# Kernel tuning notes

Measured on AMD Instinct MI355X. Metric: run time of the kernel, lower is better.

The kernel has to match this reference:

```python
import jax, jax.numpy as jnp
import numpy as np

B, N, H, L = 8, 256, 128, 3
NF, EF, TD, FH = 6, 15, 4, 64  # node feat, edge feat, temporal dim, flow hidden


def setup_inputs() -> dict:
    key = jax.random.key(0)
    ks = jax.random.split(key, 16)
    s = 0.05
    return {
        "node_features": jax.random.normal(ks[0], (B, N, NF), jnp.float32),
        "edge_features": jax.random.normal(ks[1], (B, N, N, EF), jnp.float32),
        "temporal_features": jax.random.normal(ks[2], (B, N, N, TD), jnp.float32),
        "adjacency": jax.random.randint(ks[3], (N, N), 0, 2, jnp.int32),
        "W_emb": jax.random.normal(ks[4], (NF, H), jnp.float32) * s,
        "b_emb": jnp.zeros((H,), jnp.float32),
        "msg_W": jax.random.normal(ks[5], (L, H + 3, H), jnp.float32) * s,
        "msg_b": jnp.zeros((L, H), jnp.float32),
        "upd_W": jax.random.normal(ks[6], (L, 2 * H, H), jnp.float32) * s,
        "upd_b": jnp.zeros((L, H), jnp.float32),
        "W1": jax.random.normal(ks[7], (2 * H + 3 + TD, FH), jnp.float32) * s,
        "b1": jnp.zeros((FH,), jnp.float32),
        "W2": jax.random.normal(ks[8], (FH, 1), jnp.float32) * s,
        "b2": jnp.zeros((1,), jnp.float32),
    }


def reference(node_features, edge_features, temporal_features, adjacency,
              W_emb, b_emb, msg_W, msg_b, upd_W, upd_b, W1, b1, W2, b2):
    # mask[j, i] = 1 if node i is a neighbor of node j (adjacency[j] > 0)
    mask = (adjacency > 0).astype(node_features.dtype)          # [N, N]
    deg = mask.sum(axis=1)                                      # [N]
    edge_rel = edge_features[..., -3:]                          # [B, N, N, 3]
    # aggregated relation features per destination j: sum_i mask[j,i] * edge_rel[b,i,j,:]
    r_agg = jnp.einsum('ji,bijc->bjc', mask, edge_rel)          # [B, N, 3]

    # node embedding (dropout = identity in eval)
    emb = jax.nn.relu(node_features @ W_emb + b_emb)            # [B, N, H]

    for l in range(L):
        We, Wr = msg_W[l, :H], msg_W[l, H:]                     # [H,H], [3,H]
        # msg_nn is linear, so the masked sum decomposes exactly:
        # messages[b,j] = sum_i mask[j,i]*(emb_i @ We + r_ij @ Wr + b)
        messages = (jnp.einsum('ji,bih->bjh', mask, emb @ We)
                    + r_agg @ Wr
                    + deg[None, :, None] * msg_b[l])            # [B, N, H]
        emb = jax.nn.relu(
            jnp.concatenate([emb, messages], axis=-1) @ upd_W[l] + upd_b[l])

    # pairwise flow MLP, first Linear split by input blocks [emb_i, emb_j, r, t]
    Wi, Wj = W1[:H], W1[H:2 * H]
    Wr1, Wt = W1[2 * H:2 * H + 3], W1[2 * H + 3:]
    hi = emb @ Wi                                               # [B, N, FH]
    hj = emb @ Wj                                               # [B, N, FH]
    h = jax.nn.relu(hi[:, :, None, :] + hj[:, None, :, :]
                    + edge_rel @ Wr1 + temporal_features @ Wt + b1)  # [B,N,N,FH]
    flows = jax.nn.relu(h @ W2 + b2)[..., 0]                    # [B, N, N]
    return flows
```

## Files before the change

kernel.cpp:

```cpp
#include <hip/hip_runtime.h>

#define B 8
#define N 256
#define H 128
#define NF 6
#define EF 15
#define TD 4
#define FH 64
#define M (B*N)

typedef unsigned short u16;
using short8  = __attribute__((ext_vector_type(8))) short;
using short4v = __attribute__((ext_vector_type(4))) short;
using f32x4   = __attribute__((ext_vector_type(4))) float;

__device__ __forceinline__ u16 f2bf(float x) {
    unsigned u = __float_as_uint(x);
    u += 0x7fffu + ((u >> 16) & 1u);
    return (u16)(u >> 16);
}
__device__ __forceinline__ float bf2f(u16 h) {
    return __uint_as_float(((unsigned)h) << 16);
}

__global__ void k_prep(const float* __restrict__ msg_W, const float* __restrict__ upd_W,
                       const float* __restrict__ W1,
                       u16* __restrict__ WeTh, u16* __restrict__ WeTl,
                       u16* __restrict__ UwTh, u16* __restrict__ UwTl,
                       u16* __restrict__ W1Th, u16* __restrict__ W1Tl) {
    int idx = blockIdx.x * 256 + threadIdx.x;
    float v; u16 *dh, *dl; int d;
    if (idx < 3 * 16384) {
        int l = idx / 16384, r = idx & 16383;
        int c = r >> 7, h = r & 127;
        v = msg_W[l * ((H + 3) * H) + h * H + c];
        dh = WeTh; dl = WeTl; d = idx;
    } else if (idx < 3 * 16384 + 3 * 32768) {
        int r0 = idx - 3 * 16384;
        int l = r0 / 32768, r = r0 & 32767;
        int c = r >> 8, k = r & 255;
        v = upd_W[l * (2 * H * H) + k * H + c];
        dh = UwTh; dl = UwTl; d = r0;
    } else {
        int r0 = idx - 3 * 16384 - 3 * 32768;
        int f = r0 >> 8, k = r0 & 255;
        v = W1[k * FH + f];
        dh = W1Th; dl = W1Tl; d = r0;
    }
    u16 h = f2bf(v);
    dh[d] = h;
    dl[d] = f2bf(v - bf2f(h));
}

__global__ __launch_bounds__(512) void k_init(
    const int* __restrict__ adj, const float* __restrict__ nf,
    const float* __restrict__ Wemb, const float* __restrict__ bemb,
    float* __restrict__ deg, float* __restrict__ maskT, float* __restrict__ ragg,
    u16* __restrict__ eRh, u16* __restrict__ eRl,
    u16* __restrict__ eTh, u16* __restrict__ eTl)
{
    __shared__ float red[4];
    __shared__ __align__(16) float sout[16][132];
    int t = threadIdx.x;
    if (blockIdx.x < 256) {
        int x = blockIdx.x;
        if (t < 256) {
            float v = (adj[x * N + t] > 0) ? 1.f : 0.f;
            for (int o = 32; o > 0; o >>= 1) v += __shfl_down(v, o);
            if ((t & 63) == 0) red[t >> 6] = v;
            maskT[x * N + t] = (adj[t * N + x] > 0) ? 1.f : 0.f;
            if (t < 24) ragg[x * 24 + t] = 0.f;
        }
        __syncthreads();
        if (t == 0) deg[x] = red[0] + red[1] + red[2] + red[3];
    } else {
        int tile = blockIdx.x - 256;
        int row = t >> 5, h0 = (t & 31) * 4;
        int gr = tile * 16 + row;
        float xv[NF];
#pragma unroll
        for (int k = 0; k < NF; ++k) xv[k] = nf[gr * NF + k];
#pragma unroll
        for (int c = 0; c < 4; ++c) {
            float a = bemb[h0 + c];
#pragma unroll
            for (int k = 0; k < NF; ++k) a += xv[k] * Wemb[k * H + h0 + c];
            sout[row][h0 + c] = fmaxf(a, 0.f);
        }
        __syncthreads();
        {
            float4 v = *(const float4*)&sout[row][h0];
            short4v ph, pl;
            float xs[4] = {v.x, v.y, v.z, v.w};
#pragma unroll
            for (int c = 0; c < 4; ++c) {
                u16 h = f2bf(xs[c]);
                ph[c] = (short)h;
                pl[c] = (short)f2bf(xs[c] - bf2f(h));
            }
            *(short4v*)&eRh[(size_t)gr * H + h0] = ph;
            *(short4v*)&eRl[(size_t)gr * H + h0] = pl;
        }
        {
            int hh = t >> 2, jj = (t & 3) * 4;
            short4v th, tl;
#pragma unroll
            for (int r = 0; r < 4; ++r) {
                float x = sout[jj + r][hh];
                u16 h = f2bf(x);
                th[r] = (short)h;
                tl[r] = (short)f2bf(x - bf2f(h));
            }
            size_t o = (size_t)(tile >> 4) * H * N + (size_t)hh * N + ((tile & 15) * 16) + jj;
            *(short4v*)&eTh[o] = th;
            *(short4v*)&eTl[o] = tl;
        }
    }
}

__global__ void k_erel(const float* __restrict__ edge, const float* __restrict__ maskT,
                       float* __restrict__ e0p, float* __restrict__ e1p,
                       float* __restrict__ e2p, float* __restrict__ ragg) {
    int blk = blockIdx.x;
    int b = blk >> 5, ic = blk & 31;
    int j = threadIdx.x;
    float r0 = 0.f, r1 = 0.f, r2 = 0.f;
#pragma unroll
    for (int ii = 0; ii < 8; ++ii) {
        int i = ic * 8 + ii;
        size_t base = ((size_t)(b * N + i)) * N + j;
        const float* e = edge + base * EF + (EF - 3);
        float e0 = e[0], e1 = e[1], e2 = e[2];
        e0p[base] = e0; e1p[base] = e1; e2p[base] = e2;
        float m = maskT[i * N + j];
        r0 += m * e0; r1 += m * e1; r2 += m * e2;
    }
    float* r = ragg + ((size_t)(b * N) + j) * 3;
    atomicAdd(r + 0, r0);
    atomicAdd(r + 1, r1);
    atomicAdd(r + 2, r2);
}

template <bool LAST>
__global__ __launch_bounds__(512) void k_layer(
    const u16* __restrict__ embR_hi, const u16* __restrict__ embR_lo,
    const u16* __restrict__ embT_hi, const u16* __restrict__ embT_lo,
    const int* __restrict__ adj, const float* __restrict__ ragg,
    const float* __restrict__ deg,
    const u16* __restrict__ WeT_hi, const u16* __restrict__ WeT_lo,
    const float* __restrict__ mwl, const float* __restrict__ mbl,
    const u16* __restrict__ UwT_hi, const u16* __restrict__ UwT_lo,
    const float* __restrict__ ubl,
    u16* __restrict__ oR_hi, u16* __restrict__ oR_lo,
    u16* __restrict__ oT_hi, u16* __restrict__ oT_lo,
    const u16* __restrict__ W1T_hi, const u16* __restrict__ W1T_lo,
    float* __restrict__ hi_out, float* __restrict__ hj_out)
{
    __shared__ __align__(16) u16 sbt[2][2][128][40];
    __shared__ __align__(16) u16 smask[16][264];
    __shared__ __align__(16) u16 semb_hi[16][136], semb_lo[16][136];
    __shared__ __align__(16) u16 sagg_hi[16][136], sagg_lo[16][136];
    __shared__ __align__(16) u16 smsg_hi[16][136], smsg_lo[16][136];
    __shared__ __align__(16) float sout[16][132];

    const int t = threadIdx.x;
    const int wave = t >> 6, lane = t & 63;
    const int lrow = lane & 15;
    const int kg8  = (lane >> 4) * 8;
    const int rb   = (lane >> 4) * 4;
    const int cb   = wave * 16;
    const int blk  = blockIdx.x;
    const int b    = blk >> 4, tile = blk & 15;
    const int j0   = tile * 16;
    const int gb   = b * N;

    const int sp = t >> 8, task = t & 255;
    const int sh = task >> 2, sseg = (task & 3) * 8;

    short8 r0, r1;

    {
        int j = t >> 5, i0 = (t & 31) * 8;
        int4 a0 = *(const int4*)(adj + (j0 + j) * N + i0);
        int4 a1 = *(const int4*)(adj + (j0 + j) * N + i0 + 4);
        short8 mrow;
        mrow[0] = (a0.x > 0) ? (short)0x3F80 : (short)0;
        mrow[1] = (a0.y > 0) ? (short)0x3F80 : (short)0;
        mrow[2] = (a0.z > 0) ? (short)0x3F80 : (short)0;
        mrow[3] = (a0.w > 0) ? (short)0x3F80 : (short)0;
        mrow[4] = (a1.x > 0) ? (short)0x3F80 : (short)0;
        mrow[5] = (a1.y > 0) ? (short)0x3F80 : (short)0;
        mrow[6] = (a1.z > 0) ? (short)0x3F80 : (short)0;
        mrow[7] = (a1.w > 0) ? (short)0x3F80 : (short)0;
        *(short8*)&smask[j][i0] = mrow;
        int h0 = (t & 31) * 4;
        *(short4v*)&semb_hi[j][h0] = *(const short4v*)&embR_hi[(size_t)(gb + j0 + j) * H + h0];
        *(short4v*)&semb_lo[j][h0] = *(const short4v*)&embR_lo[(size_t)(gb + j0 + j) * H + h0];
    }

    const u16* sA_hi = embT_hi + (size_t)b * H * N;
    const u16* sA_lo = embT_lo + (size_t)b * H * N;

    auto LD = [&](const u16* srcHi, const u16* srcLo, int rs, int ko) {
        const u16* s = sp ? srcLo : srcHi;
        r0 = *(const short8*)(s + (size_t)sh * rs + ko + sseg);
        r1 = *(const short8*)(s + (size_t)(sh + 64) * rs + ko + sseg);
    };
    auto WR = [&](int buf) {
        *(short8*)&sbt[buf][sp][sh][sseg] = r0;
        *(short8*)&sbt[buf][sp][sh + 64][sseg] = r1;
    };

    f32x4 acc = {0.f, 0.f, 0.f, 0.f};
    LD(sA_hi, sA_lo, N, 0);
    WR(0);
    __syncthreads();
    for (int c = 0; c < 8; ++c) {
        if (c < 7) LD(sA_hi, sA_lo, N, (c + 1) * 32);
        short8 am = *(const short8*)&smask[lrow][c * 32 + kg8];
        short8 bh = *(const short8*)&sbt[c & 1][0][cb + lrow][kg8];
        short8 bl = *(const short8*)&sbt[c & 1][1][cb + lrow][kg8];
        acc = __builtin_amdgcn_mfma_f32_16x16x32_bf16(am, bh, acc, 0, 0, 0);
        acc = __builtin_amdgcn_mfma_f32_16x16x32_bf16(am, bl, acc, 0, 0, 0);
        if (c < 7) WR((c + 1) & 1);
        __syncthreads();
    }
#pragma unroll
    for (int r = 0; r < 4; ++r) {
        float v = acc[r];
        u16 h = f2bf(v);
        sagg_hi[rb + r][cb + lrow] = h;
        sagg_lo[rb + r][cb + lrow] = f2bf(v - bf2f(h));
    }

    acc = (f32x4){0.f, 0.f, 0.f, 0.f};
    LD(WeT_hi, WeT_lo, H, 0);
    WR(0);
    __syncthreads();
    for (int c = 0; c < 4; ++c) {
        if (c < 3) LD(WeT_hi, WeT_lo, H, (c + 1) * 32);
        short8 ah = *(const short8*)&sagg_hi[lrow][c * 32 + kg8];
        short8 al = *(const short8*)&sagg_lo[lrow][c * 32 + kg8];
        short8 bh = *(const short8*)&sbt[c & 1][0][cb + lrow][kg8];
        short8 bl = *(const short8*)&sbt[c & 1][1][cb + lrow][kg8];
        acc = __builtin_amdgcn_mfma_f32_16x16x32_bf16(ah, bh, acc, 0, 0, 0);
        acc = __builtin_amdgcn_mfma_f32_16x16x32_bf16(ah, bl, acc, 0, 0, 0);
        acc = __builtin_amdgcn_mfma_f32_16x16x32_bf16(al, bh, acc, 0, 0, 0);
        if (c < 3) WR((c + 1) & 1);
        __syncthreads();
    }
    {
        int hp = cb + lrow;
        float w0 = mwl[(H + 0) * H + hp];
        float w1 = mwl[(H + 1) * H + hp];
        float w2 = mwl[(H + 2) * H + hp];
        float mb = mbl[hp];
#pragma unroll
        for (int r = 0; r < 4; ++r) {
            int jl = j0 + rb + r;
            const float* ra = ragg + (size_t)(gb + jl) * 3;
            float v = acc[r] + deg[jl] * mb + ra[0] * w0 + ra[1] * w1 + ra[2] * w2;
            u16 h = f2bf(v);
            smsg_hi[rb + r][hp] = h;
            smsg_lo[rb + r][hp] = f2bf(v - bf2f(h));
        }
    }

    acc = (f32x4){0.f, 0.f, 0.f, 0.f};
    LD(UwT_hi, UwT_lo, 2 * H, 0);
    WR(0);
    __syncthreads();
    for (int c = 0; c < 8; ++c) {
        if (c < 7) LD(UwT_hi, UwT_lo, 2 * H, (c + 1) * 32);
        int kc = (c & 3) * 32 + kg8;
        short8 ah, al;
        if (c < 4) {
            ah = *(const short8*)&semb_hi[lrow][kc];
            al = *(const short8*)&semb_lo[lrow][kc];
        } else {
            ah = *(const short8*)&smsg_hi[lrow][kc];
            al = *(const short8*)&smsg_lo[lrow][kc];
        }
        short8 bh = *(const short8*)&sbt[c & 1][0][cb + lrow][kg8];
        short8 bl = *(const short8*)&sbt[c & 1][1][cb + lrow][kg8];
        acc = __builtin_amdgcn_mfma_f32_16x16x32_bf16(ah, bh, acc, 0, 0, 0);
        acc = __builtin_amdgcn_mfma_f32_16x16x32_bf16(ah, bl, acc, 0, 0, 0);
        acc = __builtin_amdgcn_mfma_f32_16x16x32_bf16(al, bh, acc, 0, 0, 0);
        if (c < 7) WR((c + 1) & 1);
        __syncthreads();
    }
    {
        float ub = ubl[cb + lrow];
#pragma unroll
        for (int r = 0; r < 4; ++r) {
            float v = fmaxf(acc[r] + ub, 0.f);
            if constexpr (LAST) {
                u16 h = f2bf(v);
                sagg_hi[rb + r][cb + lrow] = h;
                sagg_lo[rb + r][cb + lrow] = f2bf(v - bf2f(h));
            } else {
                sout[rb + r][cb + lrow] = v;
            }
        }
    }
    __syncthreads();

    if constexpr (!LAST) {
        {
            int row = t >> 5, h0 = (t & 31) * 4;
            int gr = gb + j0 + row;
            float4 v = *(const float4*)&sout[row][h0];
            float xs[4] = {v.x, v.y, v.z, v.w};
            short4v ph, pl;
#pragma unroll
            for (int c = 0; c < 4; ++c) {
                u16 h = f2bf(xs[c]);
                ph[c] = (short)h;
                pl[c] = (short)f2bf(xs[c] - bf2f(h));
            }
            *(short4v*)&oR_hi[(size_t)gr * H + h0] = ph;
            *(short4v*)&oR_lo[(size_t)gr * H + h0] = pl;
        }
        {
            int hh = t >> 2, jj = (t & 3) * 4;
            short4v th, tl;
#pragma unroll
            for (int r = 0; r < 4; ++r) {
                float x = sout[jj + r][hh];
                u16 h = f2bf(x);
                th[r] = (short)h;
                tl[r] = (short)f2bf(x - bf2f(h));
            }
            size_t o = (size_t)b * H * N + (size_t)hh * N + j0 + jj;
            *(short4v*)&oT_hi[o] = th;
            *(short4v*)&oT_lo[o] = tl;
        }
    } else {
        acc = (f32x4){0.f, 0.f, 0.f, 0.f};
        auto LDD = [&](int ko) {
            const u16* s = sp ? W1T_lo : W1T_hi;
            r0 = *(const short8*)(s + (size_t)sh * 256 + ko + sseg);
            r1 = *(const short8*)(s + (size_t)sh * 256 + 128 + ko + sseg);
        };
        LDD(0);
        WR(0);
        __syncthreads();
        const int br = ((wave >= 4) ? 64 : 0) + (wave & 3) * 16 + lrow;
        for (int c = 0; c < 4; ++c) {
            if (c < 3) LDD((c + 1) * 32);
            short8 ah = *(const short8*)&sagg_hi[lrow][c * 32 + kg8];
            short8 al = *(const short8*)&sagg_lo[lrow][c * 32 + kg8];
            short8 bh = *(const short8*)&sbt[c & 1][0][br][kg8];
            short8 bl = *(const short8*)&sbt[c & 1][1][br][kg8];
            acc = __builtin_amdgcn_mfma_f32_16x16x32_bf16(ah, bh, acc, 0, 0, 0);
            acc = __builtin_amdgcn_mfma_f32_16x16x32_bf16(ah, bl, acc, 0, 0, 0);
            acc = __builtin_amdgcn_mfma_f32_16x16x32_bf16(al, bh, acc, 0, 0, 0);
            if (c < 3) WR((c + 1) & 1);
            __syncthreads();
        }
        int colc = ((wave >= 4) ? 64 : 0) + (wave & 3) * 16 + lrow;
#pragma unroll
        for (int r = 0; r < 4; ++r) sout[rb + r][colc] = acc[r];
        __syncthreads();
        int row = t >> 5, c0 = (t & 31) * 4;
        int gr = gb + j0 + row;
        float4 v = *(const float4*)&sout[row][c0];
        if (c0 < 64) *(float4*)&hi_out[(size_t)gr * FH + c0] = v;
        else         *(float4*)&hj_out[(size_t)gr * FH + (c0 - 64)] = v;
    }
}

__global__ __launch_bounds__(256) void k_final(
    const float* __restrict__ hi, const float* __restrict__ hj,
    const float* __restrict__ e0p, const float* __restrict__ e1p,
    const float* __restrict__ e2p, const float* __restrict__ temporal,
    const float* __restrict__ W1, const float* __restrict__ b1,
    const float* __restrict__ W2, const float* __restrict__ b2,
    float* __restrict__ flows) {
    __shared__ float his[8][FH];
    __shared__ float hjs[32][FH + 2];
    __shared__ float wr0[FH], wr1[FH], wr2[FH];
    __shared__ float wt0[FH], wt1[FH], wt2[FH], wt3[FH], bb[FH], w2s[FH];
    int blk = blockIdx.x;
    int jt = blk & 7, it = (blk >> 3) & 31, b = blk >> 8;
    int tid = threadIdx.x;
#pragma unroll
    for (int u = 0; u < 2; ++u) {
        int idx = u * 256 + tid;
        his[idx >> 6][idx & 63] = hi[((size_t)(b * N) + it * 8 + (idx >> 6)) * FH + (idx & 63)];
    }
#pragma unroll
    for (int u = 0; u < 8; ++u) {
        int idx = u * 256 + tid;
        hjs[idx >> 6][idx & 63] = hj[((size_t)(b * N) + jt * 32 + (idx >> 6)) * FH + (idx & 63)];
    }
    {
        int f = tid & 63, g = tid >> 6;
        if (g == 0) { wr0[f] = W1[(2 * H + 0) * FH + f]; wt0[f] = W1[(2 * H + 3) * FH + f]; bb[f] = b1[f]; }
        if (g == 1) { wr1[f] = W1[(2 * H + 1) * FH + f]; wt1[f] = W1[(2 * H + 4) * FH + f]; w2s[f] = W2[f]; }
        if (g == 2) { wr2[f] = W1[(2 * H + 2) * FH + f]; wt2[f] = W1[(2 * H + 5) * FH + f]; }
        if (g == 3) { wt3[f] = W1[(2 * H + 6) * FH + f]; }
    }
    __syncthreads();
    int ti = tid >> 5, tj = tid & 31;
    int i = it * 8 + ti, j = jt * 32 + tj;
    size_t pij = ((size_t)(b * N) + i) * N + j;
    float e0 = e0p[pij], e1 = e1p[pij], e2 = e2p[pij];
    float4 tf = *(const float4*)(temporal + pij * TD);
    float acc = 0.f;
#pragma unroll 8
    for (int f = 0; f < FH; ++f) {
        float v = his[ti][f] + hjs[tj][f] + bb[f]
                + e0 * wr0[f] + e1 * wr1[f] + e2 * wr2[f]
                + tf.x * wt0[f] + tf.y * wt1[f] + tf.z * wt2[f] + tf.w * wt3[f];
        acc += fmaxf(v, 0.f) * w2s[f];
    }
    flows[pij] = fmaxf(acc + b2[0], 0.f);
}

extern "C" void kernel_launch(void* const* d_in, const int* in_sizes, int n_in,
                              void* d_out, int out_size, void* d_ws, size_t ws_size,
                              hipStream_t stream) {
    const float* nf       = (const float*)d_in[0];
    const float* edge     = (const float*)d_in[1];
    const float* temporal = (const float*)d_in[2];
    const int*   adj      = (const int*)d_in[3];
    const float* W_emb    = (const float*)d_in[4];
    const float* b_emb    = (const float*)d_in[5];
    const float* msg_W    = (const float*)d_in[6];
    const float* msg_b    = (const float*)d_in[7];
    const float* upd_W    = (const float*)d_in[8];
    const float* upd_b    = (const float*)d_in[9];
    const float* W1       = (const float*)d_in[10];
    const float* b1       = (const float*)d_in[11];
    const float* W2       = (const float*)d_in[12];
    const float* b2       = (const float*)d_in[13];
    float* out = (float*)d_out;
    (void)in_sizes; (void)n_in; (void)out_size; (void)ws_size;

    char* p = (char*)d_ws;
    auto take = [&](size_t bytes) { char* r = p; p += (bytes + 255) & ~(size_t)255; return r; };
    float* deg   = (float*)take(256 * 4);
    float* ragg  = (float*)take((size_t)M * 3 * 4);
    float* maskT = (float*)take((size_t)N * N * 4);
    float* e0p   = (float*)take((size_t)B * N * N * 4);
    float* e1p   = (float*)take((size_t)B * N * N * 4);
    float* e2p   = (float*)take((size_t)B * N * N * 4);
    float* hi    = (float*)take((size_t)M * FH * 4);
    float* hj    = (float*)take((size_t)M * FH * 4);
    u16* eRhA = (u16*)take((size_t)M * H * 2);
    u16* eRlA = (u16*)take((size_t)M * H * 2);
    u16* eThA = (u16*)take((size_t)M * H * 2);
    u16* eTlA = (u16*)take((size_t)M * H * 2);
    u16* eRhB = (u16*)take((size_t)M * H * 2);
    u16* eRlB = (u16*)take((size_t)M * H * 2);
    u16* eThB = (u16*)take((size_t)M * H * 2);
    u16* eTlB = (u16*)take((size_t)M * H * 2);
    u16* WeTh = (u16*)take(3 * 16384 * 2);
    u16* WeTl = (u16*)take(3 * 16384 * 2);
    u16* UwTh = (u16*)take(3 * 32768 * 2);
    u16* UwTl = (u16*)take(3 * 32768 * 2);
    u16* W1Th = (u16*)take(16384 * 2);
    u16* W1Tl = (u16*)take(16384 * 2);

    k_prep<<<640, 256, 0, stream>>>(msg_W, upd_W, W1, WeTh, WeTl, UwTh, UwTl, W1Th, W1Tl);
    k_init<<<384, 512, 0, stream>>>(adj, nf, W_emb, b_emb, deg, maskT, ragg,
                                    eRhA, eRlA, eThA, eTlA);
    k_erel<<<256, 256, 0, stream>>>(edge, maskT, e0p, e1p, e2p, ragg);

    const int mwS = (H + 3) * H;
    k_layer<false><<<128, 512, 0, stream>>>(
        eRhA, eRlA, eThA, eTlA, adj, ragg, deg,
        WeTh + 0 * 16384, WeTl + 0 * 16384, msg_W + 0 * mwS, msg_b + 0 * H,
        UwTh + 0 * 32768, UwTl + 0 * 32768, upd_b + 0 * H,
        eRhB, eRlB, eThB, eTlB, W1Th, W1Tl, hi, hj);
    k_layer<false><<<128, 512, 0, stream>>>(
        eRhB, eRlB, eThB, eTlB, adj, ragg, deg,
        WeTh + 1 * 16384, WeTl + 1 * 16384, msg_W + 1 * mwS, msg_b + 1 * H,
        UwTh + 1 * 32768, UwTl + 1 * 32768, upd_b + 1 * H,
        eRhA, eRlA, eThA, eTlA, W1Th, W1Tl, hi, hj);
    k_layer<true><<<128, 512, 0, stream>>>(
        eRhA, eRlA, eThA, eTlA, adj, ragg, deg,
        WeTh + 2 * 16384, WeTl + 2 * 16384, msg_W + 2 * mwS, msg_b + 2 * H,
        UwTh + 2 * 32768, UwTl + 2 * 32768, upd_b + 2 * H,
        eRhB, eRlB, eThB, eTlB, W1Th, W1Tl, hi, hj);

    k_final<<<2048, 256, 0, stream>>>(hi, hj, e0p, e1p, e2p, temporal,
                                      W1, b1, W2, b2, out);
}
```

Measured before the change: 77.25 us.

## Merge setup kernels, stage edge reads via LDS, reduce ragg in first layer

Folds the weight prep, embedding init, degree and edge-relation kernels into one launch, cutting two launches and removing the maskT buffer. Edge rows are now loaded coalesced into shared memory before the last three channels are extracted. The atomic ragg accumulation is replaced by per-edge masked partials written to global memory and reduced in the first layer kernel. The layer GEMM loops are rewritten as a macro-based double-register pipeline that issues loads earlier. The trade-off is three extra B*N*N float buffers written and then read back.

```diff
diff --git a/kernel.cpp b/kernel.cpp
--- a/kernel.cpp
+++ b/kernel.cpp
@@ -23,129 +23,147 @@
     return __uint_as_float(((unsigned)h) << 16);
 }
 
-__global__ void k_prep(const float* __restrict__ msg_W, const float* __restrict__ upd_W,
-                       const float* __restrict__ W1,
-                       u16* __restrict__ WeTh, u16* __restrict__ WeTl,
-                       u16* __restrict__ UwTh, u16* __restrict__ UwTl,
-                       u16* __restrict__ W1Th, u16* __restrict__ W1Tl) {
-    int idx = blockIdx.x * 256 + threadIdx.x;
-    float v; u16 *dh, *dl; int d;
-    if (idx < 3 * 16384) {
-        int l = idx / 16384, r = idx & 16383;
-        int c = r >> 7, h = r & 127;
-        v = msg_W[l * ((H + 3) * H) + h * H + c];
-        dh = WeTh; dl = WeTl; d = idx;
-    } else if (idx < 3 * 16384 + 3 * 32768) {
-        int r0 = idx - 3 * 16384;
-        int l = r0 / 32768, r = r0 & 32767;
-        int c = r >> 8, k = r & 255;
-        v = upd_W[l * (2 * H * H) + k * H + c];
-        dh = UwTh; dl = UwTl; d = r0;
-    } else {
-        int r0 = idx - 3 * 16384 - 3 * 32768;
-        int f = r0 >> 8, k = r0 & 255;
-        v = W1[k * FH + f];
-        dh = W1Th; dl = W1Tl; d = r0;
-    }
-    u16 h = f2bf(v);
-    dh[d] = h;
-    dl[d] = f2bf(v - bf2f(h));
-}
-
-__global__ __launch_bounds__(512) void k_init(
-    const int* __restrict__ adj, const float* __restrict__ nf,
-    const float* __restrict__ Wemb, const float* __restrict__ bemb,
-    float* __restrict__ deg, float* __restrict__ maskT, float* __restrict__ ragg,
+__global__ __launch_bounds__(256) void k_setup(
+    const float* __restrict__ edge, const int* __restrict__ adj,
+    const float* __restrict__ nf, const float* __restrict__ Wemb,
+    const float* __restrict__ bemb,
+    const float* __restrict__ msg_W, const float* __restrict__ upd_W,
+    const float* __restrict__ W1,
+    float* __restrict__ e0p, float* __restrict__ e1p, float* __restrict__ e2p,
+    float* __restrict__ rp0, float* __restrict__ rp1, float* __restrict__ rp2,
+    float* __restrict__ deg,
+    u16* __restrict__ WeTh, u16* __restrict__ WeTl,
+    u16* __restrict__ UwTh, u16* __restrict__ UwTl,
+    u16* __restrict__ W1Th, u16* __restrict__ W1Tl,
     u16* __restrict__ eRh, u16* __restrict__ eRl,
     u16* __restrict__ eTh, u16* __restrict__ eTl)
 {
+    __shared__ __align__(16) float smem[3848];
     __shared__ float red[4];
-    __shared__ __align__(16) float sout[16][132];
-    int t = threadIdx.x;
-    if (blockIdx.x < 256) {
-        int x = blockIdx.x;
-        if (t < 256) {
-            float v = (adj[x * N + t] > 0) ? 1.f : 0.f;
-            for (int o = 32; o > 0; o >>= 1) v += __shfl_down(v, o);
-            if ((t & 63) == 0) red[t >> 6] = v;
-            maskT[x * N + t] = (adj[t * N + x] > 0) ? 1.f : 0.f;
-            if (t < 24) ragg[x * 24 + t] = 0.f;
+    const int t = threadIdx.x;
+    const int blk = blockIdx.x;
+
+    if (blk < 2048) {
+        const int i = blk & 255;
+        const float* src = edge + (size_t)blk * (N * EF);
+        float4* s4 = (float4*)smem;
+#pragma unroll
+        for (int u = 0; u < 4; ++u) {
+            int idx = t + u * 256;
+            if (idx < (N * EF) / 4) s4[idx] = *(const float4*)(src + idx * 4);
         }
         __syncthreads();
-        if (t == 0) deg[x] = red[0] + red[1] + red[2] + red[3];
-    } else {
-        int tile = blockIdx.x - 256;
-        int row = t >> 5, h0 = (t & 31) * 4;
-        int gr = tile * 16 + row;
-        float xv[NF];
-#pragma unroll
-        for (int k = 0; k < NF; ++k) xv[k] = nf[gr * NF + k];
-#pragma unroll
-        for (int c = 0; c < 4; ++c) {
-            float a = bemb[h0 + c];
-#pragma unroll
-            for (int k = 0; k < NF; ++k) a += xv[k] * Wemb[k * H + h0 + c];
-            sout[row][h0 + c] = fmaxf(a, 0.f);
+        const int j = t;
+        float e0 = smem[j * EF + 12];
+        float e1 = smem[j * EF + 13];
+        float e2 = smem[j * EF + 14];
+        size_t base = (size_t)blk * N + j;
+        e0p[base] = e0; e1p[base] = e1; e2p[base] = e2;
+        float m = (adj[j * N + i] > 0) ? 1.f : 0.f;
+        rp0[base] = m * e0; rp1[base] = m * e1; rp2[base] = m * e2;
+    } else if (blk < 2688) {
+        int idx = (blk - 2048) * 256 + t;
+        float v; u16 *dh, *dl; int d;
+        if (idx < 3 * 16384) {
+            int l = idx / 16384, r = idx & 16383;
+            int c = r >> 7, h = r & 127;
+            v = msg_W[l * ((H + 3) * H) + h * H + c];
+            dh = WeTh; dl = WeTl; d = idx;
+        } else if (idx < 3 * 16384 + 3 * 32768) {
+            int r0 = idx - 3 * 16384;
+            int l = r0 / 32768, r = r0 & 32767;
+            int c = r >> 8, k = r & 255;
+            v = upd_W[l * (2 * H * H) + k * H + c];
+            dh = UwTh; dl = UwTl; d = r0;
+        } else {
+            int r0 = idx - 3 * 16384 - 3 * 32768;
+            int f = r0 >> 8, k = r0 & 255;
+            v = W1[k * FH + f];
+            dh = W1Th; dl = W1Tl; d = r0;
+        }
+        u16 h = f2bf(v);
+        dh[d] = h;
+        dl[d] = f2bf(v - bf2f(h));
+    } else if (blk < 2816) {
+        int tile = blk - 2688;
+        float (*sout)[132] = (float(*)[132])smem;
+        {
+            int row = t >> 4, h0 = (t & 15) * 8;
+            int gr = tile * 16 + row;
+            float xv[NF];
+#pragma unroll
+            for (int k = 0; k < NF; ++k) xv[k] = nf[gr * NF + k];
+#pragma unroll
+            for (int c = 0; c < 8; ++c) {
+                float a = bemb[h0 + c];
+#pragma unroll
+                for (int k = 0; k < NF; ++k) a += xv[k] * Wemb[k * H + h0 + c];
+                sout[row][h0 + c] = fmaxf(a, 0.f);
+            }
         }
         __syncthreads();
         {
-            float4 v = *(const float4*)&sout[row][h0];
-            short4v ph, pl;
-            float xs[4] = {v.x, v.y, v.z, v.w};
-#pragma unroll
-            for (int c = 0; c < 4; ++c) {
-                u16 h = f2bf(xs[c]);
+            int row = t >> 4, h0 = (t & 15) * 8;
+            int gr = tile * 16 + row;
+            short8 ph, pl;
+#pragma unroll
+            for (int c = 0; c < 8; ++c) {
+                float x = sout[row][h0 + c];
+                u16 h = f2bf(x);
                 ph[c] = (short)h;
-                pl[c] = (short)f2bf(xs[c] - bf2f(h));
+                pl[c] = (short)f2bf(x - bf2f(h));
             }
-            *(short4v*)&eRh[(size_t)gr * H + h0] = ph;
-            *(short4v*)&eRl[(size_t)gr * H + h0] = pl;
+            *(short8*)&eRh[(size_t)gr * H + h0] = ph;
+            *(short8*)&eRl[(size_t)gr * H + h0] = pl;
         }
         {
-            int hh = t >> 2, jj = (t & 3) * 4;
-            short4v th, tl;
-#pragma unroll
-            for (int r = 0; r < 4; ++r) {
+            int hh = t >> 1, jj = (t & 1) * 8;
+            short8 th, tl;
+#pragma unroll
+            for (int r = 0; r < 8; ++r) {
                 float x = sout[jj + r][hh];
                 u16 h = f2bf(x);
                 th[r] = (short)h;
                 tl[r] = (short)f2bf(x - bf2f(h));
             }
             size_t o = (size_t)(tile >> 4) * H * N + (size_t)hh * N + ((tile & 15) * 16) + jj;
-            *(short4v*)&eTh[o] = th;
-            *(short4v*)&eTl[o] = tl;
-        }
+            *(short8*)&eTh[o] = th;
+            *(short8*)&eTl[o] = tl;
+        }
+    } else {
+        int jr = blk - 2816;
+        float v = (adj[jr * N + t] > 0) ? 1.f : 0.f;
+        for (int o = 32; o > 0; o >>= 1) v += __shfl_down(v, o);
+        if ((t & 63) == 0) red[t >> 6] = v;
+        __syncthreads();
+        if (t == 0) deg[jr] = red[0] + red[1] + red[2] + red[3];
     }
 }
 
-__global__ void k_erel(const float* __restrict__ edge, const float* __restrict__ maskT,
-                       float* __restrict__ e0p, float* __restrict__ e1p,
-                       float* __restrict__ e2p, float* __restrict__ ragg) {
-    int blk = blockIdx.x;
-    int b = blk >> 5, ic = blk & 31;
-    int j = threadIdx.x;
-    float r0 = 0.f, r1 = 0.f, r2 = 0.f;
-#pragma unroll
-    for (int ii = 0; ii < 8; ++ii) {
-        int i = ic * 8 + ii;
-        size_t base = ((size_t)(b * N + i)) * N + j;
-        const float* e = edge + base * EF + (EF - 3);
-        float e0 = e[0], e1 = e[1], e2 = e[2];
-        e0p[base] = e0; e1p[base] = e1; e2p[base] = e2;
-        float m = maskT[i * N + j];
-        r0 += m * e0; r1 += m * e1; r2 += m * e2;
-    }
-    float* r = ragg + ((size_t)(b * N) + j) * 3;
-    atomicAdd(r + 0, r0);
-    atomicAdd(r + 1, r1);
-    atomicAdd(r + 2, r2);
-}
-
-template <bool LAST>
+#define PIPE(NC, LD, COMP)                          \
+    LD(0, pA0, pA1);                                \
+    LD(1, pB0, pB1);                                \
+    WRX(0, pA0, pA1);                               \
+    __syncthreads();                                \
+    _Pragma("unroll")                               \
+    for (int c = 0; c < (NC); c += 2) {             \
+        WRX(1, pB0, pB1);                           \
+        if (c + 2 < (NC)) LD(c + 2, pA0, pA1);      \
+        COMP(c, 0);                                 \
+        __syncthreads();                            \
+        if (c + 2 < (NC)) WRX(0, pA0, pA1);         \
+        if (c + 3 < (NC)) LD(c + 3, pB0, pB1);      \
+        COMP(c + 1, 1);                             \
+        __syncthreads();                            \
+    }
+
+template <bool FIRST, bool LAST>
 __global__ __launch_bounds__(512) void k_layer(
     const u16* __restrict__ embR_hi, const u16* __restrict__ embR_lo,
     const u16* __restrict__ embT_hi, const u16* __restrict__ embT_lo,
-    const int* __restrict__ adj, const float* __restrict__ ragg,
+    const int* __restrict__ adj,
+    const float* __restrict__ rp0, const float* __restrict__ rp1,
+    const float* __restrict__ rp2, float* __restrict__ ragg,
     const float* __restrict__ deg,
     const u16* __restrict__ WeT_hi, const u16* __restrict__ WeT_lo,
     const float* __restrict__ mwl, const float* __restrict__ mbl,
@@ -162,6 +180,7 @@
     __shared__ __align__(16) u16 sagg_hi[16][136], sagg_lo[16][136];
     __shared__ __align__(16) u16 smsg_hi[16][136], smsg_lo[16][136];
     __shared__ __align__(16) float sout[16][132];
+    __shared__ float sragg[16][4];
 
     const int t = threadIdx.x;
     const int wave = t >> 6, lane = t & 63;
@@ -177,7 +196,7 @@
     const int sp = t >> 8, task = t & 255;
     const int sh = task >> 2, sseg = (task & 3) * 8;
 
-    short8 r0, r1;
+    short8 pA0, pA1, pB0, pB1;
 
     {
         int j = t >> 5, i0 = (t & 31) * 8;
@@ -198,33 +217,95 @@
         *(short4v*)&semb_lo[j][h0] = *(const short4v*)&embR_lo[(size_t)(gb + j0 + j) * H + h0];
     }
 
+    if constexpr (FIRST) {
+        int j16 = t >> 5, ic = t & 31;
+        int gj = gb + j0 + j16;
+        float s0 = 0.f, s1 = 0.f, s2 = 0.f;
+#pragma unroll
+        for (int k = 0; k < 8; ++k) {
+            size_t o = ((size_t)(gb + ic * 8 + k)) * N + (j0 + j16);
+            s0 += rp0[o]; s1 += rp1[o]; s2 += rp2[o];
+        }
+        for (int o = 16; o > 0; o >>= 1) {
+            s0 += __shfl_down(s0, o, 32);
+            s1 += __shfl_down(s1, o, 32);
+            s2 += __shfl_down(s2, o, 32);
+        }
+        if (ic == 0) {
+            sragg[j16][0] = s0; sragg[j16][1] = s1; sragg[j16][2] = s2;
+            float* rg = ragg + (size_t)gj * 3;
+            rg[0] = s0; rg[1] = s1; rg[2] = s2;
+        }
+    } else {
+        if (t < 48) sragg[t / 3][t % 3] = ragg[(size_t)(gb + j0 + t / 3) * 3 + (t % 3)];
+    }
+
     const u16* sA_hi = embT_hi + (size_t)b * H * N;
     const u16* sA_lo = embT_lo + (size_t)b * H * N;
 
-    auto LD = [&](const u16* srcHi, const u16* srcLo, int rs, int ko) {
-        const u16* s = sp ? srcLo : srcHi;
-        r0 = *(const short8*)(s + (size_t)sh * rs + ko + sseg);
-        r1 = *(const short8*)(s + (size_t)(sh + 64) * rs + ko + sseg);
-    };
-    auto WR = [&](int buf) {
-        *(short8*)&sbt[buf][sp][sh][sseg] = r0;
-        *(short8*)&sbt[buf][sp][sh + 64][sseg] = r1;
-    };
+#define WRX(buf, q0, q1)                              \
+    { *(short8*)&sbt[buf][sp][sh][sseg] = q0;         \
+      *(short8*)&sbt[buf][sp][sh + 64][sseg] = q1; }
+
+#define LDA(c, q0, q1)                                                        \
+    { const u16* s_ = sp ? sA_lo : sA_hi;                                     \
+      q0 = *(const short8*)(s_ + (size_t)sh * N + (c) * 32 + sseg);           \
+      q1 = *(const short8*)(s_ + (size_t)(sh + 64) * N + (c) * 32 + sseg); }
+
+#define LDB(c, q0, q1)                                                        \
+    { const u16* s_ = sp ? WeT_lo : WeT_hi;                                   \
+      q0 = *(const short8*)(s_ + (size_t)sh * H + (c) * 32 + sseg);           \
+      q1 = *(const short8*)(s_ + (size_t)(sh + 64) * H + (c) * 32 + sseg); }
+
+#define LDC(c, q0, q1)                                                        \
+    { const u16* s_ = sp ? UwT_lo : UwT_hi;                                   \
+      q0 = *(const short8*)(s_ + (size_t)sh * 2 * H + (c) * 32 + sseg);       \
+      q1 = *(const short8*)(s_ + (size_t)(sh + 64) * 2 * H + (c) * 32 + sseg); }
+
+#define LDD(c, q0, q1)                                                        \
+    { const u16* s_ = sp ? W1T_lo : W1T_hi;                                   \
+      q0 = *(const short8*)(s_ + (size_t)sh * 256 + (c) * 32 + sseg);         \
+      q1 = *(const short8*)(s_ + (size_t)sh * 256 + 128 + (c) * 32 + sseg); }
+
+#define COMPA(c, buf)                                                           \
+    { short8 am = *(const short8*)&smask[lrow][(c) * 32 + kg8];                 \
+      short8 bh = *(const short8*)&sbt[buf][0][cb + lrow][kg8];                 \
+      short8 bl = *(const short8*)&sbt[buf][1][cb + lrow][kg8];                 \
+      acc = __builtin_amdgcn_mfma_f32_16x16x32_bf16(am, bh, acc, 0, 0, 0);      \
+      acc = __builtin_amdgcn_mfma_f32_16x16x32_bf16(am, bl, acc, 0, 0, 0); }
+
+#define COMPB(c, buf)                                                           \
+    { short8 ah = *(const short8*)&sagg_hi[lrow][(c) * 32 + kg8];               \
+      short8 al = *(const short8*)&sagg_lo[lrow][(c) * 32 + kg8];               \
+      short8 bh = *(const short8*)&sbt[buf][0][cb + lrow][kg8];                 \
+      short8 bl = *(const short8*)&sbt[buf][1][cb + lrow][kg8];                 \
+      acc = __builtin_amdgcn_mfma_f32_16x16x32_bf16(ah, bh, acc, 0, 0, 0);      \
+      acc = __builtin_amdgcn_mfma_f32_16x16x32_bf16(ah, bl, acc, 0, 0, 0);      \
+      acc = __builtin_amdgcn_mfma_f32_16x16x32_bf16(al, bh, acc, 0, 0, 0); }
+
+#define COMPC(c, buf)                                                           \
+    { int kc = ((c) & 3) * 32 + kg8; short8 ah, al;                             \
+      if ((c) < 4) { ah = *(const short8*)&semb_hi[lrow][kc];                   \
+                     al = *(const short8*)&semb_lo[lrow][kc]; }                 \
+      else         { ah = *(const short8*)&smsg_hi[lrow][kc];                   \
+                     al = *(const short8*)&smsg_lo[lrow][kc]; }                 \
+      short8 bh = *(const short8*)&sbt[buf][0][cb + lrow][kg8];                 \
+      short8 bl = *(const short8*)&sbt[buf][1][cb + lrow][kg8];                 \
+      acc = __builtin_amdgcn_mfma_f32_16x16x32_bf16(ah, bh, acc, 0, 0, 0);      \
+      acc = __builtin_amdgcn_mfma_f32_16x16x32_bf16(ah, bl, acc, 0, 0, 0);      \
+      acc = __builtin_amdgcn_mfma_f32_16x16x32_bf16(al, bh, acc, 0, 0, 0); }
+
+#define COMPD(c, buf)                                                           \
+    { short8 ah = *(const short8*)&sagg_hi[lrow][(c) * 32 + kg8];               \
+      short8 al = *(const short8*)&sagg_lo[lrow][(c) * 32 + kg8];               \
+      short8 bh = *(const short8*)&sbt[buf][0][br][kg8];                        \
+      short8 bl = *(const short8*)&sbt[buf][1][br][kg8];                        \
+      acc = __builtin_amdgcn_mfma_f32_16x16x32_bf16(ah, bh, acc, 0, 0, 0);      \
+      acc = __builtin_amdgcn_mfma_f32_16x16x32_bf16(ah, bl, acc, 0, 0, 0);      \
+      acc = __builtin_amdgcn_mfma_f32_16x16x32_bf16(al, bh, acc, 0, 0, 0); }
 
     f32x4 acc = {0.f, 0.f, 0.f, 0.f};
-    LD(sA_hi, sA_lo, N, 0);
-    WR(0);
-    __syncthreads();
-    for (int c = 0; c < 8; ++c) {
-        if (c < 7) LD(sA_hi, sA_lo, N, (c + 1) * 32);
-        short8 am = *(const short8*)&smask[lrow][c * 32 + kg8];
-        short8 bh = *(const short8*)&sbt[c & 1][0][cb + lrow][kg8];
-        short8 bl = *(const short8*)&sbt[c & 1][1][cb + lrow][kg8];
-        acc = __builtin_amdgcn_mfma_f32_16x16x32_bf16(am, bh, acc, 0, 0, 0);
-        acc = __builtin_amdgcn_mfma_f32_16x16x32_bf16(am, bl, acc, 0, 0, 0);
-        if (c < 7) WR((c + 1) & 1);
-        __syncthreads();
-    }
+    PIPE(8, LDA, COMPA)
 #pragma unroll
     for (int r = 0; r < 4; ++r) {
         float v = acc[r];
@@ -234,21 +315,7 @@
     }
 
     acc = (f32x4){0.f, 0.f, 0.f, 0.f};
-    LD(WeT_hi, WeT_lo, H, 0);
-    WR(0);
-    __syncthreads();
-    for (int c = 0; c < 4; ++c) {
-        if (c < 3) LD(WeT_hi, WeT_lo, H, (c + 1) * 32);
-        short8 ah = *(const short8*)&sagg_hi[lrow][c * 32 + kg8];
-        short8 al = *(const short8*)&sagg_lo[lrow][c * 32 + kg8];
-        short8 bh = *(const short8*)&sbt[c & 1][0][cb + lrow][kg8];
-        short8 bl = *(const short8*)&sbt[c & 1][1][cb + lrow][kg8];
-        acc = __builtin_amdgcn_mfma_f32_16x16x32_bf16(ah, bh, acc, 0, 0, 0);
-        acc = __builtin_amdgcn_mfma_f32_16x16x32_bf16(ah, bl, acc, 0, 0, 0);
-        acc = __builtin_amdgcn_mfma_f32_16x16x32_bf16(al, bh, acc, 0, 0, 0);
-        if (c < 3) WR((c + 1) & 1);
-        __syncthreads();
-    }
+    PIPE(4, LDB, COMPB)
     {
         int hp = cb + lrow;
         float w0 = mwl[(H + 0) * H + hp];
@@ -258,8 +325,9 @@
 #pragma unroll
         for (int r = 0; r < 4; ++r) {
             int jl = j0 + rb + r;
-            const float* ra = ragg + (size_t)(gb + jl) * 3;
-            float v = acc[r] + deg[jl] * mb + ra[0] * w0 + ra[1] * w1 + ra[2] * w2;
+            float v = acc[r] + deg[jl] * mb
+                    + sragg[rb + r][0] * w0 + sragg[rb + r][1] * w1
+                    + sragg[rb + r][2] * w2;
             u16 h = f2bf(v);
             smsg_hi[rb + r][hp] = h;
             smsg_lo[rb + r][hp] = f2bf(v - bf2f(h));
@@ -267,28 +335,7 @@
     }
 
     acc = (f32x4){0.f, 0.f, 0.f, 0.f};
-    LD(UwT_hi, UwT_lo, 2 * H, 0);
-    WR(0);
-    __syncthreads();
-    for (int c = 0; c < 8; ++c) {
-        if (c < 7) LD(UwT_hi, UwT_lo, 2 * H, (c + 1) * 32);
-        int kc = (c & 3) * 32 + kg8;
-        short8 ah, al;
-        if (c < 4) {
-            ah = *(const short8*)&semb_hi[lrow][kc];
-            al = *(const short8*)&semb_lo[lrow][kc];
-        } else {
-            ah = *(const short8*)&smsg_hi[lrow][kc];
-            al = *(const short8*)&smsg_lo[lrow][kc];
-        }
-        short8 bh = *(const short8*)&sbt[c & 1][0][cb + lrow][kg8];
-        short8 bl = *(const short8*)&sbt[c & 1][1][cb + lrow][kg8];
-        acc = __builtin_amdgcn_mfma_f32_16x16x32_bf16(ah, bh, acc, 0, 0, 0);
-        acc = __builtin_amdgcn_mfma_f32_16x16x32_bf16(ah, bl, acc, 0, 0, 0);
-        acc = __builtin_amdgcn_mfma_f32_16x16x32_bf16(al, bh, acc, 0, 0, 0);
-        if (c < 7) WR((c + 1) & 1);
-        __syncthreads();
-    }
+    PIPE(8, LDC, COMPC)
     {
         float ub = ubl[cb + lrow];
 #pragma unroll
@@ -336,31 +383,11 @@
             *(short4v*)&oT_lo[o] = tl;
         }
     } else {
+        const int br = ((wave >= 4) ? 64 : 0) + (wave & 3) * 16 + lrow;
         acc = (f32x4){0.f, 0.f, 0.f, 0.f};
-        auto LDD = [&](int ko) {
-            const u16* s = sp ? W1T_lo : W1T_hi;
-            r0 = *(const short8*)(s + (size_t)sh * 256 + ko + sseg);
-            r1 = *(const short8*)(s + (size_t)sh * 256 + 128 + ko + sseg);
-        };
-        LDD(0);
-        WR(0);
-        __syncthreads();
-        const int br = ((wave >= 4) ? 64 : 0) + (wave & 3) * 16 + lrow;
-        for (int c = 0; c < 4; ++c) {
-            if (c < 3) LDD((c + 1) * 32);
-            short8 ah = *(const short8*)&sagg_hi[lrow][c * 32 + kg8];
-            short8 al = *(const short8*)&sagg_lo[lrow][c * 32 + kg8];
-            short8 bh = *(const short8*)&sbt[c & 1][0][br][kg8];
-            short8 bl = *(const short8*)&sbt[c & 1][1][br][kg8];
-            acc = __builtin_amdgcn_mfma_f32_16x16x32_bf16(ah, bh, acc, 0, 0, 0);
-            acc = __builtin_amdgcn_mfma_f32_16x16x32_bf16(ah, bl, acc, 0, 0, 0);
-            acc = __builtin_amdgcn_mfma_f32_16x16x32_bf16(al, bh, acc, 0, 0, 0);
-            if (c < 3) WR((c + 1) & 1);
-            __syncthreads();
-        }
-        int colc = ((wave >= 4) ? 64 : 0) + (wave & 3) * 16 + lrow;
-#pragma unroll
-        for (int r = 0; r < 4; ++r) sout[rb + r][colc] = acc[r];
+        PIPE(4, LDD, COMPD)
+#pragma unroll
+        for (int r = 0; r < 4; ++r) sout[rb + r][br] = acc[r];
         __syncthreads();
         int row = t >> 5, c0 = (t & 31) * 4;
         int gr = gb + j0 + row;
@@ -368,6 +395,15 @@
         if (c0 < 64) *(float4*)&hi_out[(size_t)gr * FH + c0] = v;
         else         *(float4*)&hj_out[(size_t)gr * FH + (c0 - 64)] = v;
     }
+#undef WRX
+#undef LDA
+#undef LDB
+#undef LDC
+#undef LDD
+#undef COMPA
+#undef COMPB
+#undef COMPC
+#undef COMPD
 }
 
 __global__ __launch_bounds__(256) void k_final(
@@ -442,10 +478,12 @@
     auto take = [&](size_t bytes) { char* r = p; p += (bytes + 255) & ~(size_t)255; return r; };
     float* deg   = (float*)take(256 * 4);
     float* ragg  = (float*)take((size_t)M * 3 * 4);
-    float* maskT = (float*)take((size_t)N * N * 4);
     float* e0p   = (float*)take((size_t)B * N * N * 4);
     float* e1p   = (float*)take((size_t)B * N * N * 4);
     float* e2p   = (float*)take((size_t)B * N * N * 4);
+    float* rp0   = (float*)take((size_t)B * N * N * 4);
+    float* rp1   = (float*)take((size_t)B * N * N * 4);
+    float* rp2   = (float*)take((size_t)B * N * N * 4);
     float* hi    = (float*)take((size_t)M * FH * 4);
     float* hj    = (float*)take((size_t)M * FH * 4);
     u16* eRhA = (u16*)take((size_t)M * H * 2);
@@ -463,24 +501,25 @@
     u16* W1Th = (u16*)take(16384 * 2);
     u16* W1Tl = (u16*)take(16384 * 2);
 
-    k_prep<<<640, 256, 0, stream>>>(msg_W, upd_W, W1, WeTh, WeTl, UwTh, UwTl, W1Th, W1Tl);
-    k_init<<<384, 512, 0, stream>>>(adj, nf, W_emb, b_emb, deg, maskT, ragg,
-                                    eRhA, eRlA, eThA, eTlA);
-    k_erel<<<256, 256, 0, stream>>>(edge, maskT, e0p, e1p, e2p, ragg);
+    k_setup<<<3072, 256, 0, stream>>>(edge, adj, nf, W_emb, b_emb,
+                                      msg_W, upd_W, W1,
+                                      e0p, e1p, e2p, rp0, rp1, rp2, deg,
+                                      WeTh, WeTl, UwTh, UwTl, W1Th, W1Tl,
+                                      eRhA, eRlA, eThA, eTlA);
 
     const int mwS = (H + 3) * H;
-    k_layer<false><<<128, 512, 0, stream>>>(
-        eRhA, eRlA, eThA, eTlA, adj, ragg, deg,
+    k_layer<true, false><<<128, 512, 0, stream>>>(
+        eRhA, eRlA, eThA, eTlA, adj, rp0, rp1, rp2, ragg, deg,
         WeTh + 0 * 16384, WeTl + 0 * 16384, msg_W + 0 * mwS, msg_b + 0 * H,
         UwTh + 0 * 32768, UwTl + 0 * 32768, upd_b + 0 * H,
         eRhB, eRlB, eThB, eTlB, W1Th, W1Tl, hi, hj);
-    k_layer<false><<<128, 512, 0, stream>>>(
-        eRhB, eRlB, eThB, eTlB, adj, ragg, deg,
+    k_layer<false, false><<<128, 512, 0, stream>>>(
+        eRhB, eRlB, eThB, eTlB, adj, rp0, rp1, rp2, ragg, deg,
         WeTh + 1 * 16384, WeTl + 1 * 16384, msg_W + 1 * mwS, msg_b + 1 * H,
         UwTh + 1 * 32768, UwTl + 1 * 32768, upd_b + 1 * H,
         eRhA, eRlA, eThA, eTlA, W1Th, W1Tl, hi, hj);
-    k_layer<true><<<128, 512, 0, stream>>>(
-        eRhA, eRlA, eThA, eTlA, adj, ragg, deg,
+    k_layer<false, true><<<128, 512, 0, stream>>>(
+        eRhA, eRlA, eThA, eTlA, adj, rp0, rp1, rp2, ragg, deg,
         WeTh + 2 * 16384, WeTl + 2 * 16384, msg_W + 2 * mwS, msg_b + 2 * H,
         UwTh + 2 * 32768, UwTl + 2 * 32768, upd_b + 2 * H,
         eRhB, eRlB, eThB, eTlB, W1Th, W1Tl, hi, hj);
```

After: 73.78 us. -4.5%, faster.
